# Performance work log

Hardware: AMD Instinct MI355X
Metric: run time of the kernel (lower is better)

## Reference

```python
import jax, jax.numpy as jnp
import numpy as np

GRID_DIM = 7
NQUERIES = 100
C = 256

def setup_inputs() -> dict:
    key = jax.random.key(0)
    k1, k2 = jax.random.split(key)
    images = jax.random.normal(k1, (4, 224, 224, C), dtype=jnp.float32)
    # learned query weight (orthogonal init in original; random normal is fine as a stand-in)
    queries = jax.random.normal(k2, (NQUERIES, C), dtype=jnp.float32)
    return {"images": images, "queries": queries}

def _positions(g):
    lin = jnp.linspace(0.0, 1.0, g + 1)[:-1].astype(jnp.float32)
    # positions[i*g + j] = (lin[i], lin[j]) -> (h_frac, w_frac), row-major over the grid
    return jnp.stack(jnp.meshgrid(lin, lin, indexing="ij"), axis=-1).reshape(g * g, 2)

def reference(images, queries):
    g = GRID_DIM
    B, H, W, Cc = images.shape
    h, w = H // g, W // g
    # batch-extract all grid regions at once: [B, g*g, h*w, C]
    regions = images.reshape(B, g, h, g, w, Cc)
    regions = regions.transpose(0, 1, 3, 2, 4, 5).reshape(B, g * g, h * w, Cc)
    # keras Attention (dot, no scale): softmax(Q K^T) V, queries shared across batch/regions
    scores = jnp.einsum("qc,bnsc->bnqs", queries, regions)  # [B, g*g, nq, h*w]
    attn = jax.nn.softmax(scores, axis=-1)
    out = jnp.einsum("bnqs,bnsc->bnqc", attn, regions)  # [B, g*g, nq, C]
    return out, _positions(g)
```

## Files before the change

kernel.cpp:

```cpp
#include <hip/hip_runtime.h>
#include <stdint.h>

typedef short short8 __attribute__((ext_vector_type(8)));
typedef __fp16 fp16x8 __attribute__((ext_vector_type(8)));
typedef float f32x16 __attribute__((ext_vector_type(16)));
typedef unsigned int uint;

#define NREG 49
#define NQ   100
#define CC   256
#define OUT_POS_OFF 5017600
#define PO_PER (NQ*CC)
#define QF_BYTES 65536
#define MFMA_BF16 __builtin_amdgcn_mfma_f32_32x32x16_bf16
#define MFMA_F16  __builtin_amdgcn_mfma_f32_32x32x16_f16

union U4H8 { uint4 u; fp16x8 h; short8 s; };

#define LBAR() do { \
    asm volatile("s_waitcnt lgkmcnt(0)" ::: "memory"); \
    __builtin_amdgcn_s_barrier(); \
} while (0)

__device__ __forceinline__ uint pkrtz(float a, float b){
    auto v = __builtin_amdgcn_cvt_pkrtz(a, b);
    return __builtin_bit_cast(uint, v);
}
__device__ __forceinline__ uint16_t f2bf_rne(float x){
    uint u = __float_as_uint(x);
    u += 0x7fffu + ((u >> 16) & 1u);
    return (uint16_t)(u >> 16);
}
__device__ __forceinline__ float bf2f(uint16_t b){
    return __uint_as_float(((uint)b) << 16);
}

__global__ __launch_bounds__(512) void qfrag_kernel(const float* __restrict__ Qg,
                                                    uint4* __restrict__ qf){
    int gid  = blockIdx.x * 512 + threadIdx.x;
    int lane = gid & 63;
    int frag = gid >> 6;
    int k    = frag & 15;
    int qt   = frag >> 4;
    int q    = qt * 32 + (lane & 31);
    int c0   = k * 16 + (lane >> 5) * 8;
    float v[8];
#pragma unroll
    for (int j = 0; j < 8; ++j) v[j] = (q < NQ) ? Qg[q * CC + c0 + j] : 0.f;
    qf[gid] = make_uint4(pkrtz(v[0], v[1]), pkrtz(v[2], v[3]),
                         pkrtz(v[4], v[5]), pkrtz(v[6], v[7]));
}

__global__ __launch_bounds__(512, 2) void attn_kernel(
        const float* __restrict__ img, const uint4* __restrict__ qf,
        float* __restrict__ out, float* __restrict__ po,
        float* __restrict__ pl, int split)
{
    __shared__ __align__(16) unsigned char smem[65536];
    unsigned char* sRT = smem;
    unsigned char* sU  = smem + 32768;

    const int tid = threadIdx.x;
    const int seg = blockIdx.x % split;
    const int bn  = blockIdx.x / split;
    const int rr  = bn % NREG;
    const int bb  = bn / NREG;
    const int gh  = rr / 7, gw = rr % 7;

    if (bn == 0 && seg == 0 && tid < NREG){
        out[OUT_POS_OFF + 2 * tid]     = (float)((tid / 7) / 7.0);
        out[OUT_POS_OFF + 2 * tid + 1] = (float)((tid % 7) / 7.0);
    }

    const int lane = tid & 63, w = tid >> 6;
    const int l31  = lane & 31;
    const int st = w & 1, qt = w >> 1;
    const int mp = w & 1, cq = w >> 1;

    const int sloc = tid >> 3;
    const int ct   = tid & 7;
    const int stw  = sloc >> 5;
    const int s31  = sloc & 31;
    const int ksw  = sloc >> 4;
    const int lhw  = (sloc >> 3) & 1;
    const int jw   = sloc & 7;
    const int rtwbase = ((ksw * 8 + ct) * 64 + lhw * 32) * 16 + jw * 2;
    const int afwbase = (stw * 16 + ct * 2) * 1024 + s31 * 16;

    const float* rbase = img + ((size_t)(bb * 224 + gh * 32) * 224 + gw * 32) * CC;

    uint4 qr[16];
#pragma unroll
    for (int k = 0; k < 16; ++k) qr[k] = qf[(qt * 16 + k) * 64 + lane];

    f32x16 acc00, acc01, acc10, acc11;
#pragma unroll
    for (int i = 0; i < 16; ++i){ acc00[i]=0.f; acc01[i]=0.f; acc10[i]=0.f; acc11[i]=0.f; }
    float lp = 0.f;
    const int qq = qt * 32 + l31;

    const int nch = 16 / split;
    const int ch0 = seg * nch, ch1 = ch0 + nch;

    float4 rb[8], rb2[8], rb3[8];
    {
        int p = ch0 * 64 + sloc;
        const float* gp = rbase + ((p >> 5) * 224 + (p & 31)) * CC + ct * 32;
#pragma unroll
        for (int j = 0; j < 8; ++j) rb[j] = *(const float4*)(gp + j * 4);
    }
    if (ch0 + 1 < ch1){
        int p = (ch0 + 1) * 64 + sloc;
        const float* gp = rbase + ((p >> 5) * 224 + (p & 31)) * CC + ct * 32;
#pragma unroll
        for (int j = 0; j < 8; ++j) rb2[j] = *(const float4*)(gp + j * 4);
    }

    for (int ch = ch0; ch < ch1; ++ch){
#pragma unroll
        for (int r = 0; r < 4; ++r){
            uint4 o = make_uint4(pkrtz(rb[2*r].x,   rb[2*r].y),
                                 pkrtz(rb[2*r].z,   rb[2*r].w),
                                 pkrtz(rb[2*r+1].x, rb[2*r+1].y),
                                 pkrtz(rb[2*r+1].z, rb[2*r+1].w));
            *(uint4*)(sU + afwbase + ((r >> 1) * 1024) + ((r & 1) * 512)) = o;
        }
#pragma unroll
        for (int i = 0; i < 32; ++i){
            const float* fp = (const float*)rb;
            uint u = __float_as_uint(fp[i]);
            *(uint16_t*)(sRT + rtwbase + ((i ^ ct) << 4)) = (uint16_t)(u >> 16);
        }

        if (ch + 2 < ch1){
            int p = (ch + 2) * 64 + sloc;
            const float* gp = rbase + ((p >> 5) * 224 + (p & 31)) * CC + ct * 32;
#pragma unroll
            for (int j = 0; j < 8; ++j) rb3[j] = *(const float4*)(gp + j * 4);
        }
        LBAR();

        f32x16 a1;
#pragma unroll
        for (int i = 0; i < 16; ++i) a1[i] = 0.f;
#pragma unroll
        for (int k = 0; k < 16; ++k){
            U4H8 af; af.u = *(const uint4*)(sU + ((st * 16 + k) * 64 + lane) * 16);
            U4H8 bq; bq.u = qr[k];
            a1 = MFMA_F16(af.h, bq.h, a1, 0, 0, 0);
        }
        LBAR();

#pragma unroll
        for (int g2 = 0; g2 < 4; ++g2){
            uint16_t e[4];
#pragma unroll
            for (int r2 = 0; r2 < 4; ++r2){
                float sc = a1[g2 * 4 + r2];
                float pv = exp2f(sc * 1.4426950408889634f - 57.70780163555852f);
                e[r2] = f2bf_rne(pv);
                lp += bf2f(e[r2]);
            }
            int kst = st * 2 + (g2 >> 1);
            int boff = ((kst * 4 + qt) * 64 + (g2 & 1) * 32 + l31) * 16 + (lane >> 5) * 8;
            *(uint2*)(sU + boff) = make_uint2((uint)e[0] | ((uint)e[1] << 16),
                                              (uint)e[2] | ((uint)e[3] << 16));
        }
        LBAR();

#pragma unroll
        for (int ks = 0; ks < 4; ++ks){
            U4H8 A0, A1, B0, B1;
            A0.u = *(const uint4*)(sU  + ((ks * 4 + mp * 2    ) * 64 + lane) * 16);
            A1.u = *(const uint4*)(sU  + ((ks * 4 + mp * 2 + 1) * 64 + lane) * 16);
            B0.u = *(const uint4*)(sRT + ((ks * 8 + cq * 2    ) * 64 + (lane ^ (cq * 2    ))) * 16);
            B1.u = *(const uint4*)(sRT + ((ks * 8 + cq * 2 + 1) * 64 + (lane ^ (cq * 2 + 1))) * 16);
            acc00 = MFMA_BF16(A0.s, B0.s, acc00, 0, 0, 0);
            acc01 = MFMA_BF16(A0.s, B1.s, acc01, 0, 0, 0);
            acc10 = MFMA_BF16(A1.s, B0.s, acc10, 0, 0, 0);
            acc11 = MFMA_BF16(A1.s, B1.s, acc11, 0, 0, 0);
        }
        LBAR();

#pragma unroll
        for (int j = 0; j < 8; ++j){ rb[j] = rb2[j]; rb2[j] = rb3[j]; }
    }

    float* sL = (float*)sU;
    if (tid < 128) sL[tid] = 0.f;
    __syncthreads();
    atomicAdd(&sL[qq], lp);
    __syncthreads();

    const int c0 = cq * 64 + l31;
    if (split == 1){
        float* ob = out + (size_t)bn * PO_PER;
#pragma unroll
        for (int r = 0; r < 16; ++r){
            int row = (r & 3) + 8 * (r >> 2) + 4 * (lane >> 5);
            int q0 = mp * 64 + row, q1 = q0 + 32;
            if (q0 < NQ){
                float inv = 1.0f / sL[q0];
                ob[q0 * CC + c0]      = acc00[r] * inv;
                ob[q0 * CC + c0 + 32] = acc01[r] * inv;
            }
            if (q1 < NQ){
                float inv = 1.0f / sL[q1];
                ob[q1 * CC + c0]      = acc10[r] * inv;
                ob[q1 * CC + c0 + 32] = acc11[r] * inv;
            }
        }
    } else {
        float* ob = po + ((size_t)bn * split + seg) * PO_PER;
#pragma unroll
        for (int r = 0; r < 16; ++r){
            int row = (r & 3) + 8 * (r >> 2) + 4 * (lane >> 5);
            int q0 = mp * 64 + row, q1 = q0 + 32;
            if (q0 < NQ){
                ob[q0 * CC + c0]      = acc00[r];
                ob[q0 * CC + c0 + 32] = acc01[r];
            }
            if (q1 < NQ){
                ob[q1 * CC + c0]      = acc10[r];
                ob[q1 * CC + c0 + 32] = acc11[r];
            }
        }
        if (tid < 128) pl[((size_t)bn * split + seg) * 128 + tid] = sL[tid];
    }
}

__global__ __launch_bounds__(512) void reduce_kernel(
        const float* __restrict__ po, const float* __restrict__ pl,
        float* __restrict__ out, int split)
{
    __shared__ float sInv[64];
    const int bn = blockIdx.x >> 1, hf = blockIdx.x & 1, tid = threadIdx.x;
    if (tid < 50){
        int q = hf * 50 + tid;
        float s = 0.f;
        for (int g = 0; g < split; ++g)
            s += pl[((size_t)bn * split + g) * 128 + q];
        sInv[tid] = 1.0f / s;
    }
    __syncthreads();
    const float* base = po + (size_t)bn * split * PO_PER;
    float* ob = out + (size_t)bn * PO_PER;
#pragma unroll 1
    for (int i = 0; i < 25; ++i){
        int idx = hf * 12800 + i * 512 + tid;
        float s = 0.f;
        for (int g = 0; g < split; ++g) s += base[g * PO_PER + idx];
        ob[idx] = s * sInv[(idx >> 8) - hf * 50];
    }
}

extern "C" void kernel_launch(void* const* d_in, const int* in_sizes, int n_in,
                              void* d_out, int out_size, void* d_ws, size_t ws_size,
                              hipStream_t stream){
    const float* img = (const float*)d_in[0];
    const float* Qg  = (const float*)d_in[1];
    float* out = (float*)d_out;

    uint4* qf = (uint4*)d_ws;
    qfrag_kernel<<<8, 512, 0, stream>>>(Qg, qf);

    int split = 1;
    const size_t per_seg = (size_t)196 * (PO_PER + 128) * sizeof(float);
    if (ws_size >= QF_BYTES + 4 * per_seg) split = 4;

    float *po = nullptr, *pl = nullptr;
    if (split > 1){
        po = (float*)((char*)d_ws + QF_BYTES);
        pl = po + (size_t)196 * split * PO_PER;
    }

    attn_kernel<<<196 * split, 512, 0, stream>>>(img, qf, out, po, pl, split);
    if (split > 1)
        reduce_kernel<<<392, 512, 0, stream>>>(po, pl, out, split);
}
```

Before: 409.8 us.

## Double-buffer LDS stages to cut per-chunk barriers and overlap staging

Splits LDS into two ping-pong buffers for the fp16 key tile and the bf16 transposed value tile, plus a separate probability buffer. The next chunk is converted and written into the alternate buffer after the PV MFMAs, which cuts per-chunk barriers from four to two. Register prefetch depth drops from two chunks to one. LDS per block grows from 64KB to 144KB, so only one 512-thread block can fit per CU, halving occupancy against the launch bound of two.

```diff
diff --git a/kernel.cpp b/kernel.cpp
--- a/kernel.cpp
+++ b/kernel.cpp
@@ -56,9 +56,8 @@
         float* __restrict__ out, float* __restrict__ po,
         float* __restrict__ pl, int split)
 {
-    __shared__ __align__(16) unsigned char smem[65536];
-    unsigned char* sRT = smem;
-    unsigned char* sU  = smem + 32768;
+    __shared__ __align__(16) unsigned char smem[147456];
+    unsigned char* sP = smem + 131072;
 
     const int tid = threadIdx.x;
     const int seg = blockIdx.x % split;
@@ -102,28 +101,24 @@
     const int nch = 16 / split;
     const int ch0 = seg * nch, ch1 = ch0 + nch;
 
-    float4 rb[8], rb2[8], rb3[8];
+    float4 rb[8];
     {
         int p = ch0 * 64 + sloc;
         const float* gp = rbase + ((p >> 5) * 224 + (p & 31)) * CC + ct * 32;
 #pragma unroll
         for (int j = 0; j < 8; ++j) rb[j] = *(const float4*)(gp + j * 4);
     }
-    if (ch0 + 1 < ch1){
-        int p = (ch0 + 1) * 64 + sloc;
-        const float* gp = rbase + ((p >> 5) * 224 + (p & 31)) * CC + ct * 32;
-#pragma unroll
-        for (int j = 0; j < 8; ++j) rb2[j] = *(const float4*)(gp + j * 4);
-    }
-
-    for (int ch = ch0; ch < ch1; ++ch){
+
+    {
+        unsigned char* sAf = smem;
+        unsigned char* sRT = smem + 65536;
 #pragma unroll
         for (int r = 0; r < 4; ++r){
             uint4 o = make_uint4(pkrtz(rb[2*r].x,   rb[2*r].y),
                                  pkrtz(rb[2*r].z,   rb[2*r].w),
                                  pkrtz(rb[2*r+1].x, rb[2*r+1].y),
                                  pkrtz(rb[2*r+1].z, rb[2*r+1].w));
-            *(uint4*)(sU + afwbase + ((r >> 1) * 1024) + ((r & 1) * 512)) = o;
+            *(uint4*)(sAf + afwbase + ((r >> 1) * 1024) + ((r & 1) * 512)) = o;
         }
 #pragma unroll
         for (int i = 0; i < 32; ++i){
@@ -131,13 +126,21 @@
             uint u = __float_as_uint(fp[i]);
             *(uint16_t*)(sRT + rtwbase + ((i ^ ct) << 4)) = (uint16_t)(u >> 16);
         }
-
-        if (ch + 2 < ch1){
-            int p = (ch + 2) * 64 + sloc;
+        if (ch0 + 1 < ch1){
+            int p = (ch0 + 1) * 64 + sloc;
             const float* gp = rbase + ((p >> 5) * 224 + (p & 31)) * CC + ct * 32;
 #pragma unroll
-            for (int j = 0; j < 8; ++j) rb3[j] = *(const float4*)(gp + j * 4);
-        }
+            for (int j = 0; j < 8; ++j) rb[j] = *(const float4*)(gp + j * 4);
+        }
+    }
+
+    int par = 0;
+    for (int ch = ch0; ch < ch1; ++ch){
+        unsigned char* sAf = smem + (par << 15);
+        unsigned char* sRT = smem + 65536 + (par << 15);
+        unsigned char* sAfN = smem + ((par ^ 1) << 15);
+        unsigned char* sRTN = smem + 65536 + ((par ^ 1) << 15);
+
         LBAR();
 
         f32x16 a1;
@@ -145,11 +148,10 @@
         for (int i = 0; i < 16; ++i) a1[i] = 0.f;
 #pragma unroll
         for (int k = 0; k < 16; ++k){
-            U4H8 af; af.u = *(const uint4*)(sU + ((st * 16 + k) * 64 + lane) * 16);
+            U4H8 af; af.u = *(const uint4*)(sAf + ((st * 16 + k) * 64 + lane) * 16);
             U4H8 bq; bq.u = qr[k];
             a1 = MFMA_F16(af.h, bq.h, a1, 0, 0, 0);
         }
-        LBAR();
 
 #pragma unroll
         for (int g2 = 0; g2 < 4; ++g2){
@@ -163,16 +165,17 @@
             }
             int kst = st * 2 + (g2 >> 1);
             int boff = ((kst * 4 + qt) * 64 + (g2 & 1) * 32 + l31) * 16 + (lane >> 5) * 8;
-            *(uint2*)(sU + boff) = make_uint2((uint)e[0] | ((uint)e[1] << 16),
+            *(uint2*)(sP + boff) = make_uint2((uint)e[0] | ((uint)e[1] << 16),
                                               (uint)e[2] | ((uint)e[3] << 16));
         }
+
         LBAR();
 
 #pragma unroll
         for (int ks = 0; ks < 4; ++ks){
             U4H8 A0, A1, B0, B1;
-            A0.u = *(const uint4*)(sU  + ((ks * 4 + mp * 2    ) * 64 + lane) * 16);
-            A1.u = *(const uint4*)(sU  + ((ks * 4 + mp * 2 + 1) * 64 + lane) * 16);
+            A0.u = *(const uint4*)(sP  + ((ks * 4 + mp * 2    ) * 64 + lane) * 16);
+            A1.u = *(const uint4*)(sP  + ((ks * 4 + mp * 2 + 1) * 64 + lane) * 16);
             B0.u = *(const uint4*)(sRT + ((ks * 8 + cq * 2    ) * 64 + (lane ^ (cq * 2    ))) * 16);
             B1.u = *(const uint4*)(sRT + ((ks * 8 + cq * 2 + 1) * 64 + (lane ^ (cq * 2 + 1))) * 16);
             acc00 = MFMA_BF16(A0.s, B0.s, acc00, 0, 0, 0);
@@ -180,13 +183,35 @@
             acc10 = MFMA_BF16(A1.s, B0.s, acc10, 0, 0, 0);
             acc11 = MFMA_BF16(A1.s, B1.s, acc11, 0, 0, 0);
         }
-        LBAR();
-
-#pragma unroll
-        for (int j = 0; j < 8; ++j){ rb[j] = rb2[j]; rb2[j] = rb3[j]; }
-    }
-
-    float* sL = (float*)sU;
+
+        if (ch + 1 < ch1){
+#pragma unroll
+            for (int r = 0; r < 4; ++r){
+                uint4 o = make_uint4(pkrtz(rb[2*r].x,   rb[2*r].y),
+                                     pkrtz(rb[2*r].z,   rb[2*r].w),
+                                     pkrtz(rb[2*r+1].x, rb[2*r+1].y),
+                                     pkrtz(rb[2*r+1].z, rb[2*r+1].w));
+                *(uint4*)(sAfN + afwbase + ((r >> 1) * 1024) + ((r & 1) * 512)) = o;
+            }
+#pragma unroll
+            for (int i = 0; i < 32; ++i){
+                const float* fp = (const float*)rb;
+                uint u = __float_as_uint(fp[i]);
+                *(uint16_t*)(sRTN + rtwbase + ((i ^ ct) << 4)) = (uint16_t)(u >> 16);
+            }
+            if (ch + 2 < ch1){
+                int p = (ch + 2) * 64 + sloc;
+                const float* gp = rbase + ((p >> 5) * 224 + (p & 31)) * CC + ct * 32;
+#pragma unroll
+                for (int j = 0; j < 8; ++j) rb[j] = *(const float4*)(gp + j * 4);
+            }
+        }
+        par ^= 1;
+    }
+
+    __syncthreads();
+
+    float* sL = (float*)sP;
     if (tid < 128) sL[tid] = 0.f;
     __syncthreads();
     atomicAdd(&sL[qq], lp);
```

New measurement: 376.0 us. 8.3% less time.
